# Kernel optimization log

Measured on AMD Instinct MI355X. Metric: run time of the kernel, lower is better.

Reference implementation:

```python
import jax, jax.numpy as jnp
import numpy as np

B, T, D, S, DEPTH, MAX_TOK = 2048, 64, 512, 64, 2, 64
LN_EPS = 1e-5


def setup_inputs() -> dict:
    key = jax.random.key(0)
    ks = jax.random.split(key, 9)
    sc = lambda k, shp, s: (jax.random.normal(k, shp, jnp.float32) * s)
    return {
        "tokens": jax.random.normal(ks[0], (B, T, D), jnp.float32),
        "pos_emb": sc(ks[1], (MAX_TOK, D), 0.02),          # nn.Embedding(max_tokens, dim)
        "A_log": sc(ks[2], (DEPTH, S), 0.5),               # log of state decay rates
        "Wd": sc(ks[3], (DEPTH, D, S), D ** -0.5),         # delta (selectivity) projection
        "bd": jnp.zeros((DEPTH, S), jnp.float32),
        "Wb": sc(ks[4], (DEPTH, D, S), D ** -0.5),         # input->state projection (B)
        "bb": jnp.zeros((DEPTH, S), jnp.float32),
        "Wc": sc(ks[5], (DEPTH, S, D), S ** -0.5),         # state->output projection (C)
        "bc": jnp.zeros((DEPTH, D), jnp.float32),
        "Dp": jnp.ones((DEPTH, D), jnp.float32),           # skip/pass-through gain D
        "Ws": sc(ks[6], (DEPTH, S, D), S ** -0.5),         # state_to_shot Linear weights
        "bs": jnp.zeros((DEPTH, D), jnp.float32),
        "gamma": jnp.ones((D,), jnp.float32),              # LayerNorm
        "beta": jnp.zeros((D,), jnp.float32),
    }


def _selective_scan(x, A_log, Wd, bd, Wb, bb, Wc, bc, Dp):
    """Selective SSM layer: per-token input-dependent decay + drive, vector state.

    x: [B, T, D] -> (y: [B, T, D], final_state: [B, S])
    """
    delta = jax.nn.softplus(jnp.einsum('btd,ds->bts', x, Wd) + bd)   # [B,T,S]
    decay = jnp.exp(-delta * jnp.exp(A_log))                          # [B,T,S]
    drive = delta * (jnp.einsum('btd,ds->bts', x, Wb) + bb)          # [B,T,S]

    def step(h, inp):
        dec, u = inp
        h = dec * h + u
        return h, h

    h0 = jnp.zeros((x.shape[0], decay.shape[-1]), x.dtype)
    hT, hs = jax.lax.scan(step, h0, (decay.transpose(1, 0, 2), drive.transpose(1, 0, 2)))
    hs = hs.transpose(1, 0, 2)                                        # [B,T,S]
    y = jnp.einsum('bts,sd->btd', hs, Wc) + bc + x * Dp
    return y, hT


def reference(tokens, pos_emb, A_log, Wd, bd, Wb, bb, Wc, bc, Dp, Ws, bs, gamma, beta):
    t = tokens.shape[1]
    hidden = tokens + pos_emb[:t][None]                               # add position embedding
    depth = A_log.shape[0]
    shot_state = None
    for i in range(depth):  # small fixed depth
        hidden, shot_state = _selective_scan(hidden, A_log[i], Wd[i], bd[i], Wb[i], bb[i], Wc[i], bc[i], Dp[i])
        hidden = hidden + (shot_state @ Ws[i] + bs[i])[:, None, :]
    pooled = hidden.mean(axis=1) + shot_state @ Ws[-1] + bs[-1]       # [B, D]
    mu = pooled.mean(-1, keepdims=True)
    var = ((pooled - mu) ** 2).mean(-1, keepdims=True)
    shot = (pooled - mu) / jnp.sqrt(var + LN_EPS) * gamma + beta
    return hidden, shot
```

## Files before the change

kernel.cpp:

```cpp
#include <hip/hip_runtime.h>
#include <hip/hip_bf16.h>
#include <math.h>

typedef __attribute__((ext_vector_type(8))) short bf16x8;
typedef __attribute__((ext_vector_type(4))) float f32x4;

#define NB 2048
#define NT 64
#define ND 512
#define NS 64
#define NTH 512
#define LN_EPS 1e-5f

#define XH_B    0
#define HS_B    65536
#define SCANF_B 73728
#define HT_B    73984
#define STM_B   74240
#define RED_B   76288
#define LDS_BYTES 76416

#define BB_OFF  65536
#define BC_OFF  131072
#define WS_OFF  196608
#define POS_OFF 262144
#define PACK_ELEMS 294912

__device__ __forceinline__ unsigned short f2b(float x) {
    __hip_bfloat16 h = __float2bfloat16(x);
    return *(unsigned short*)&h;
}
__device__ __forceinline__ float b2f(unsigned short u) {
    __hip_bfloat16 h; *(unsigned short*)&h = u;
    return __bfloat162float(h);
}
__device__ __forceinline__ int xh_off(int t, int cb) { return t * 1024 + (cb ^ ((t & 15) << 4)); }
__device__ __forceinline__ int hs_off(int t, int cb) { return t * 128  + (cb ^ ((t & 7)  << 4)); }

__global__ void prep_pack(const float* __restrict__ Wd, const float* __restrict__ Wb,
                          const float* __restrict__ Wc, const float* __restrict__ Ws,
                          const float* __restrict__ pos_emb,
                          unsigned short* __restrict__ pack) {
    int i = blockIdx.x * 256 + threadIdx.x;
    if (i >= PACK_ELEMS) return;
    float v;
    if (i >= POS_OFF) {
        v = pos_emb[i - POS_OFF];
    } else {
        int which = i >> 16;
        int r = i & 0xFFFF;
        if (which < 2) {
            int j = r & 7, l = (r >> 3) & 63, ks = (r >> 9) & 15, nt = (r >> 13) & 3, dep = r >> 15;
            int s = nt * 16 + (l & 15);
            int k = ks * 32 + (l >> 4) * 8 + j;
            const float* W = which ? Wb : Wd;
            v = W[(dep * 512 + k) * 64 + s];
        } else if (which == 2) {
            int j = r & 7, l = (r >> 3) & 63, ks = (r >> 9) & 1, ntg = (r >> 10) & 31, dep = r >> 15;
            int d = ntg * 16 + (l & 15);
            int k = ks * 32 + (l >> 4) * 8 + j;
            v = Wc[(dep * 64 + k) * 512 + d];
        } else {
            int dep = r >> 15, rem = r & 0x7FFF;
            v = Ws[dep * (NS * ND) + rem];
        }
    }
    pack[i] = f2b(v);
}

__global__ __launch_bounds__(NTH, 4)
void ssm_mfma(const float* __restrict__ tokens,
              const float* __restrict__ A_log,
              const float* __restrict__ bd, const float* __restrict__ bb,
              const float* __restrict__ bc, const float* __restrict__ Dp,
              const float* __restrict__ bs,
              const float* __restrict__ gma, const float* __restrict__ bta,
              const unsigned short* __restrict__ pack,
              float* __restrict__ out_hidden, float* __restrict__ out_shot)
{
    extern __shared__ char sm[];
    float* scanF = (float*)(sm + SCANF_B);
    float* hT    = (float*)(sm + HT_B);
    float* stm   = (float*)(sm + STM_B);
    float* red   = (float*)(sm + RED_B);

    const int tid  = threadIdx.x;
    const int b    = blockIdx.x;
    const int lane = tid & 63;
    const int w    = tid >> 6;
    const int lr   = lane & 15;
    const int lg   = lane >> 4;
    const int nt   = w & 3;
    const int mh   = w >> 2;

    {
        const f32x4*   tp = (const f32x4*)(tokens + (size_t)b * (NT * ND));
        const ushort4* pp = (const ushort4*)(pack + POS_OFF);
        #pragma unroll
        for (int i = 0; i < 16; ++i) {
            int f = i * NTH + tid;
            f32x4 a = __builtin_nontemporal_load(&tp[f]);
            ushort4 p = pp[f];
            int row = f >> 7, cb = (f & 127) * 8;
            ushort4 q;
            q.x = f2b(a.x + b2f(p.x));
            q.y = f2b(a.y + b2f(p.y));
            q.z = f2b(a.z + b2f(p.z));
            q.w = f2b(a.w + b2f(p.w));
            *(ushort4*)(sm + XH_B + xh_off(row, cb)) = q;
        }
    }
    __syncthreads();

    for (int dep = 0; dep < 2; ++dep) {
        f32x4 accD[2] = {f32x4{0,0,0,0}, f32x4{0,0,0,0}};
        f32x4 accB[2] = {f32x4{0,0,0,0}, f32x4{0,0,0,0}};
        {
            const unsigned short* BdP = pack + (dep * 4 + nt) * 8192;
            const unsigned short* BbP = BdP + BB_OFF;
            const int rowA0 = 32 * mh + lr;
            const int rowA1 = rowA0 + 16;
            #pragma unroll 4
            for (int ks = 0; ks < 16; ++ks) {
                int cb = ks * 64 + lg * 16;
                bf16x8 a0 = *(const bf16x8*)(sm + XH_B + xh_off(rowA0, cb));
                bf16x8 a1 = *(const bf16x8*)(sm + XH_B + xh_off(rowA1, cb));
                bf16x8 b0 = *(const bf16x8*)(BdP + ks * 512 + lane * 8);
                bf16x8 b1 = *(const bf16x8*)(BbP + ks * 512 + lane * 8);
                accD[0] = __builtin_amdgcn_mfma_f32_16x16x32_bf16(a0, b0, accD[0], 0, 0, 0);
                accD[1] = __builtin_amdgcn_mfma_f32_16x16x32_bf16(a1, b0, accD[1], 0, 0, 0);
                accB[0] = __builtin_amdgcn_mfma_f32_16x16x32_bf16(a0, b1, accB[0], 0, 0, 0);
                accB[1] = __builtin_amdgcn_mfma_f32_16x16x32_bf16(a1, b1, accB[1], 0, 0, 0);
            }
        }
        const int scol = nt * 16 + lr;
        float dcy[8], u[8];
        {
            float bdv = bd[dep * 64 + scol];
            float bbv = bb[dep * 64 + scol];
            float eA  = __expf(A_log[dep * 64 + scol]);
            #pragma unroll
            for (int m = 0; m < 2; ++m)
                #pragma unroll
                for (int r = 0; r < 4; ++r) {
                    float dpre  = accD[m][r] + bdv;
                    float delta = (dpre > 20.f) ? dpre : log1pf(__expf(dpre));
                    dcy[m * 4 + r] = __expf(-delta * eA);
                    u[m * 4 + r]   = delta * (accB[m][r] + bbv);
                }
        }
        float F[2], P[2];
        #pragma unroll
        for (int m = 0; m < 2; ++m) {
            float h = 0.f, p = 1.f;
            #pragma unroll
            for (int r = 0; r < 4; ++r) { h = fmaf(dcy[m * 4 + r], h, u[m * 4 + r]); p *= dcy[m * 4 + r]; }
            F[m] = h; P[m] = p;
        }
        float hin_lo = 0.f, hin_hi = 0.f;
        if (mh == 0) {
            float hin = 0.f;
            #pragma unroll
            for (int j = 0; j < 8; ++j) {
                float Fj = __shfl(j < 4 ? F[0] : F[1], (j & 3) * 16 + lr, 64);
                float Pj = __shfl(j < 4 ? P[0] : P[1], (j & 3) * 16 + lr, 64);
                if (j == lg)     hin_lo = hin;
                if (j == 4 + lg) hin_hi = hin;
                hin = fmaf(Pj, hin, Fj);
            }
            if (lg == 0) scanF[scol] = hin;
        }
        __syncthreads();
        if (mh == 1) {
            float hin = scanF[scol];
            #pragma unroll
            for (int j = 0; j < 8; ++j) {
                float Fj = __shfl(j < 4 ? F[0] : F[1], (j & 3) * 16 + lr, 64);
                float Pj = __shfl(j < 4 ? P[0] : P[1], (j & 3) * 16 + lr, 64);
                if (j == lg)     hin_lo = hin;
                if (j == 4 + lg) hin_hi = hin;
                hin = fmaf(Pj, hin, Fj);
            }
        }
        #pragma unroll
        for (int m = 0; m < 2; ++m) {
            float h = m ? hin_hi : hin_lo;
            #pragma unroll
            for (int r = 0; r < 4; ++r) {
                h = fmaf(dcy[m * 4 + r], h, u[m * 4 + r]);
                int t = 32 * mh + 16 * m + 4 * lg + r;
                *(unsigned short*)(sm + HS_B + hs_off(t, scol * 2)) = f2b(h);
            }
            if (m == 1 && mh == 1 && lg == 3) hT[scol] = h;
        }
        __syncthreads();

        {
            const unsigned short* WsP = pack + WS_OFF + dep * (NS * ND);
            float acc = bs[dep * ND + tid];
            #pragma unroll 8
            for (int s = 0; s < 64; ++s) acc = fmaf(hT[s], b2f(WsP[s * ND + tid]), acc);
            stm[tid] = acc;
        }

        f32x4 accC[4][4];
        #pragma unroll
        for (int tt = 0; tt < 4; ++tt)
            #pragma unroll
            for (int dt = 0; dt < 4; ++dt) accC[tt][dt] = f32x4{0, 0, 0, 0};
        {
            const unsigned short* WcA = pack + BC_OFF + (dep * 32 + w * 4) * 1024;
            #pragma unroll
            for (int ks = 0; ks < 2; ++ks) {
                bf16x8 hfr[4];
                #pragma unroll
                for (int tt = 0; tt < 4; ++tt)
                    hfr[tt] = *(const bf16x8*)(sm + HS_B + hs_off(tt * 16 + lr, ks * 64 + lg * 16));
                #pragma unroll
                for (int dt = 0; dt < 4; ++dt) {
                    bf16x8 wfr = *(const bf16x8*)(WcA + (dt * 2 + ks) * 512 + lane * 8);
                    #pragma unroll
                    for (int tt = 0; tt < 4; ++tt)
                        accC[tt][dt] = __builtin_amdgcn_mfma_f32_16x16x32_bf16(wfr, hfr[tt], accC[tt][dt], 0, 0, 0);
                }
            }
        }
        __syncthreads();

        {
            const float* bcd = bc + dep * ND;
            const float* Dpd = Dp + dep * ND;
            f32x4 psumv[4] = {f32x4{0,0,0,0}, f32x4{0,0,0,0}, f32x4{0,0,0,0}, f32x4{0,0,0,0}};
            #pragma unroll
            for (int tt = 0; tt < 4; ++tt) {
                int t = tt * 16 + lr;
                #pragma unroll
                for (int dt = 0; dt < 4; ++dt) {
                    int d0 = w * 64 + dt * 16 + 4 * lg;
                    ushort4 xq = *(const ushort4*)(sm + XH_B + xh_off(t, d0 * 2));
                    f32x4 bc4 = *(const f32x4*)&bcd[d0];
                    f32x4 dp4 = *(const f32x4*)&Dpd[d0];
                    f32x4 st4 = *(const f32x4*)&stm[d0];
                    f32x4 v4;
                    v4.x = accC[tt][dt].x + bc4.x + b2f(xq.x) * dp4.x + st4.x;
                    v4.y = accC[tt][dt].y + bc4.y + b2f(xq.y) * dp4.y + st4.y;
                    v4.z = accC[tt][dt].z + bc4.z + b2f(xq.z) * dp4.z + st4.z;
                    v4.w = accC[tt][dt].w + bc4.w + b2f(xq.w) * dp4.w + st4.w;
                    if (dep == 0) {
                        ushort4 q;
                        q.x = f2b(v4.x); q.y = f2b(v4.y); q.z = f2b(v4.z); q.w = f2b(v4.w);
                        *(ushort4*)(sm + XH_B + xh_off(t, d0 * 2)) = q;
                    } else {
                        __builtin_nontemporal_store(v4, (f32x4*)&out_hidden[((size_t)b * NT + t) * ND + d0]);
                        psumv[dt] += v4;
                    }
                }
            }
            if (dep == 1) {
                #pragma unroll
                for (int dt = 0; dt < 4; ++dt)
                    #pragma unroll
                    for (int c = 0; c < 4; ++c) {
                        float v = psumv[dt][c];
                        v += __shfl_xor(v, 1, 64);
                        v += __shfl_xor(v, 2, 64);
                        v += __shfl_xor(v, 4, 64);
                        v += __shfl_xor(v, 8, 64);
                        psumv[dt][c] = v;
                    }
                if (lr == 0) {
                    #pragma unroll
                    for (int dt = 0; dt < 4; ++dt) {
                        int d0 = w * 64 + dt * 16 + 4 * lg;
                        f32x4 st4 = *(const f32x4*)&stm[d0];
                        f32x4 nv = psumv[dt] * (1.0f / 64.0f) + st4;
                        *(f32x4*)&stm[d0] = nv;
                    }
                }
            }
        }
        __syncthreads();
    }

    float pv = stm[tid];
    float s1 = pv, s2 = pv * pv;
    #pragma unroll
    for (int off = 32; off; off >>= 1) {
        s1 += __shfl_down(s1, off, 64);
        s2 += __shfl_down(s2, off, 64);
    }
    if (lane == 0) { red[w] = s1; red[8 + w] = s2; }
    __syncthreads();
    if (tid == 0) {
        float a = 0.f, q = 0.f;
        for (int i = 0; i < 8; ++i) { a += red[i]; q += red[8 + i]; }
        float mu = a * (1.0f / ND);
        float var = q * (1.0f / ND) - mu * mu;
        red[16] = mu;
        red[17] = rsqrtf(var + LN_EPS);
    }
    __syncthreads();
    out_shot[(size_t)b * ND + tid] = (pv - red[16]) * red[17] * gma[tid] + bta[tid];
}

extern "C" void kernel_launch(void* const* d_in, const int* in_sizes, int n_in,
                              void* d_out, int out_size, void* d_ws, size_t ws_size,
                              hipStream_t stream) {
    const float* tokens  = (const float*)d_in[0];
    const float* pos_emb = (const float*)d_in[1];
    const float* A_log   = (const float*)d_in[2];
    const float* Wd      = (const float*)d_in[3];
    const float* bd      = (const float*)d_in[4];
    const float* Wb      = (const float*)d_in[5];
    const float* bb      = (const float*)d_in[6];
    const float* Wc      = (const float*)d_in[7];
    const float* bc      = (const float*)d_in[8];
    const float* Dp      = (const float*)d_in[9];
    const float* Ws      = (const float*)d_in[10];
    const float* bs      = (const float*)d_in[11];
    const float* gma     = (const float*)d_in[12];
    const float* bta     = (const float*)d_in[13];

    unsigned short* pack = (unsigned short*)d_ws;
    float* out_hidden = (float*)d_out;
    float* out_shot   = (float*)d_out + (size_t)NB * NT * ND;

    prep_pack<<<(PACK_ELEMS + 255) / 256, 256, 0, stream>>>(Wd, Wb, Wc, Ws, pos_emb, pack);

    (void)hipFuncSetAttribute((const void*)ssm_mfma,
                              hipFuncAttributeMaxDynamicSharedMemorySize,
                              (int)LDS_BYTES);
    ssm_mfma<<<NB, NTH, LDS_BYTES, stream>>>(
        tokens, A_log, bd, bb, bc, Dp, bs, gma, bta,
        pack, out_hidden, out_shot);
}
```

Baseline: 278.7 us.

## Fold state-to-shot broadcast into Wc MFMA as extra K-steps, fuse biases

The per-layer hT@Ws broadcast term is folded into the Wc MFMA by extending K from 64 to 128. The extra K-steps use the last hidden state row replicated across tiles, with the weights packed into a combined fragment layout. bc+bs is pre-summed in the prep kernel, the per-thread scalar Ws loop only runs for the final pooled term, and one barrier is moved. It also swaps log1pf for a fast __logf(1+exp) and uses a nontemporal store for the shot output. This doubles the MFMA count for the Wc stage but removes a serial 64-step scalar loop and LDS traffic, and the fast log is slightly less precise for very negative inputs.

```diff
diff --git a/kernel.cpp b/kernel.cpp
--- a/kernel.cpp
+++ b/kernel.cpp
@@ -20,11 +20,12 @@
 #define RED_B   76288
 #define LDS_BYTES 76416
 
-#define BB_OFF  65536
-#define BC_OFF  131072
-#define WS_OFF  196608
-#define POS_OFF 262144
-#define PACK_ELEMS 294912
+#define BB_OFF   65536
+#define FRAG_OFF 131072
+#define WSL_OFF  262144
+#define POS_OFF  294912
+#define BCF_OFF  327680
+#define PREP_TOTAL 328704
 
 __device__ __forceinline__ unsigned short f2b(float x) {
     __hip_bfloat16 h = __float2bfloat16(x);
@@ -40,30 +41,34 @@
 __global__ void prep_pack(const float* __restrict__ Wd, const float* __restrict__ Wb,
                           const float* __restrict__ Wc, const float* __restrict__ Ws,
                           const float* __restrict__ pos_emb,
+                          const float* __restrict__ bc, const float* __restrict__ bs,
                           unsigned short* __restrict__ pack) {
     int i = blockIdx.x * 256 + threadIdx.x;
-    if (i >= PACK_ELEMS) return;
+    if (i >= PREP_TOTAL) return;
+    if (i >= BCF_OFF) {
+        int f = i - BCF_OFF;
+        ((float*)(pack + BCF_OFF))[f] = bc[f] + bs[f];
+        return;
+    }
     float v;
-    if (i >= POS_OFF) {
+    if (i < BB_OFF) {
+        int j = i & 7, l = (i >> 3) & 63, ks = (i >> 9) & 15, nt = (i >> 13) & 3, dep = (i >> 15) & 1;
+        v = Wd[((size_t)dep * 512 + ks * 32 + (l >> 4) * 8 + j) * 64 + nt * 16 + (l & 15)];
+    } else if (i < FRAG_OFF) {
+        int r = i - BB_OFF;
+        int j = r & 7, l = (r >> 3) & 63, ks = (r >> 9) & 15, nt = (r >> 13) & 3, dep = (r >> 15) & 1;
+        v = Wb[((size_t)dep * 512 + ks * 32 + (l >> 4) * 8 + j) * 64 + nt * 16 + (l & 15)];
+    } else if (i < WSL_OFF) {
+        int r = i - FRAG_OFF;
+        int j = r & 7, l = (r >> 3) & 63, ks = (r >> 9) & 3, ntg = (r >> 11) & 31, dep = (r >> 16) & 1;
+        int d = ntg * 16 + (l & 15);
+        int kk = (l >> 4) * 8 + j;
+        if (ks < 2) v = Wc[((size_t)dep * 64 + ks * 32 + kk) * 512 + d];
+        else        v = Ws[((size_t)dep * 64 + (ks - 2) * 32 + kk) * 512 + d];
+    } else if (i < POS_OFF) {
+        v = Ws[32768 + (i - WSL_OFF)];
+    } else {
         v = pos_emb[i - POS_OFF];
-    } else {
-        int which = i >> 16;
-        int r = i & 0xFFFF;
-        if (which < 2) {
-            int j = r & 7, l = (r >> 3) & 63, ks = (r >> 9) & 15, nt = (r >> 13) & 3, dep = r >> 15;
-            int s = nt * 16 + (l & 15);
-            int k = ks * 32 + (l >> 4) * 8 + j;
-            const float* W = which ? Wb : Wd;
-            v = W[(dep * 512 + k) * 64 + s];
-        } else if (which == 2) {
-            int j = r & 7, l = (r >> 3) & 63, ks = (r >> 9) & 1, ntg = (r >> 10) & 31, dep = r >> 15;
-            int d = ntg * 16 + (l & 15);
-            int k = ks * 32 + (l >> 4) * 8 + j;
-            v = Wc[(dep * 64 + k) * 512 + d];
-        } else {
-            int dep = r >> 15, rem = r & 0x7FFF;
-            v = Ws[dep * (NS * ND) + rem];
-        }
     }
     pack[i] = f2b(v);
 }
@@ -72,7 +77,7 @@
 void ssm_mfma(const float* __restrict__ tokens,
               const float* __restrict__ A_log,
               const float* __restrict__ bd, const float* __restrict__ bb,
-              const float* __restrict__ bc, const float* __restrict__ Dp,
+              const float* __restrict__ Dp,
               const float* __restrict__ bs,
               const float* __restrict__ gma, const float* __restrict__ bta,
               const unsigned short* __restrict__ pack,
@@ -144,7 +149,7 @@
                 #pragma unroll
                 for (int r = 0; r < 4; ++r) {
                     float dpre  = accD[m][r] + bdv;
-                    float delta = (dpre > 20.f) ? dpre : log1pf(__expf(dpre));
+                    float delta = (dpre > 20.f) ? dpre : __logf(1.f + __expf(dpre));
                     dcy[m * 4 + r] = __expf(-delta * eA);
                     u[m * 4 + r]   = delta * (accB[m][r] + bbv);
                 }
@@ -195,40 +200,45 @@
         }
         __syncthreads();
 
-        {
-            const unsigned short* WsP = pack + WS_OFF + dep * (NS * ND);
-            float acc = bs[dep * ND + tid];
-            #pragma unroll 8
-            for (int s = 0; s < 64; ++s) acc = fmaf(hT[s], b2f(WsP[s * ND + tid]), acc);
-            stm[tid] = acc;
-        }
-
         f32x4 accC[4][4];
         #pragma unroll
         for (int tt = 0; tt < 4; ++tt)
             #pragma unroll
             for (int dt = 0; dt < 4; ++dt) accC[tt][dt] = f32x4{0, 0, 0, 0};
         {
-            const unsigned short* WcA = pack + BC_OFF + (dep * 32 + w * 4) * 1024;
-            #pragma unroll
-            for (int ks = 0; ks < 2; ++ks) {
+            const unsigned short* WcA = pack + FRAG_OFF + (dep * 32 + w * 4) * 2048;
+            #pragma unroll
+            for (int ks = 0; ks < 4; ++ks) {
                 bf16x8 hfr[4];
-                #pragma unroll
-                for (int tt = 0; tt < 4; ++tt)
-                    hfr[tt] = *(const bf16x8*)(sm + HS_B + hs_off(tt * 16 + lr, ks * 64 + lg * 16));
+                if (ks < 2) {
+                    #pragma unroll
+                    for (int tt = 0; tt < 4; ++tt)
+                        hfr[tt] = *(const bf16x8*)(sm + HS_B + hs_off(tt * 16 + lr, ks * 64 + lg * 16));
+                } else {
+                    bf16x8 hb = *(const bf16x8*)(sm + HS_B + hs_off(63, (ks - 2) * 64 + lg * 16));
+                    #pragma unroll
+                    for (int tt = 0; tt < 4; ++tt) hfr[tt] = hb;
+                }
                 #pragma unroll
                 for (int dt = 0; dt < 4; ++dt) {
-                    bf16x8 wfr = *(const bf16x8*)(WcA + (dt * 2 + ks) * 512 + lane * 8);
+                    bf16x8 wfr = *(const bf16x8*)(WcA + dt * 2048 + ks * 512 + lane * 8);
                     #pragma unroll
                     for (int tt = 0; tt < 4; ++tt)
                         accC[tt][dt] = __builtin_amdgcn_mfma_f32_16x16x32_bf16(wfr, hfr[tt], accC[tt][dt], 0, 0, 0);
                 }
             }
         }
-        __syncthreads();
+
+        if (dep == 1) {
+            const unsigned short* WsL = pack + WSL_OFF;
+            float acc = bs[512 + tid];
+            #pragma unroll 8
+            for (int s = 0; s < 64; ++s) acc = fmaf(hT[s], b2f(WsL[s * 512 + tid]), acc);
+            stm[tid] = acc;
+        }
 
         {
-            const float* bcd = bc + dep * ND;
+            const float* bcf = (const float*)(pack + BCF_OFF) + dep * ND;
             const float* Dpd = Dp + dep * ND;
             f32x4 psumv[4] = {f32x4{0,0,0,0}, f32x4{0,0,0,0}, f32x4{0,0,0,0}, f32x4{0,0,0,0}};
             #pragma unroll
@@ -238,14 +248,13 @@
                 for (int dt = 0; dt < 4; ++dt) {
                     int d0 = w * 64 + dt * 16 + 4 * lg;
                     ushort4 xq = *(const ushort4*)(sm + XH_B + xh_off(t, d0 * 2));
-                    f32x4 bc4 = *(const f32x4*)&bcd[d0];
+                    f32x4 bc4 = *(const f32x4*)&bcf[d0];
                     f32x4 dp4 = *(const f32x4*)&Dpd[d0];
-                    f32x4 st4 = *(const f32x4*)&stm[d0];
                     f32x4 v4;
-                    v4.x = accC[tt][dt].x + bc4.x + b2f(xq.x) * dp4.x + st4.x;
-                    v4.y = accC[tt][dt].y + bc4.y + b2f(xq.y) * dp4.y + st4.y;
-                    v4.z = accC[tt][dt].z + bc4.z + b2f(xq.z) * dp4.z + st4.z;
-                    v4.w = accC[tt][dt].w + bc4.w + b2f(xq.w) * dp4.w + st4.w;
+                    v4.x = accC[tt][dt].x + bc4.x + b2f(xq.x) * dp4.x;
+                    v4.y = accC[tt][dt].y + bc4.y + b2f(xq.y) * dp4.y;
+                    v4.z = accC[tt][dt].z + bc4.z + b2f(xq.z) * dp4.z;
+                    v4.w = accC[tt][dt].w + bc4.w + b2f(xq.w) * dp4.w;
                     if (dep == 0) {
                         ushort4 q;
                         q.x = f2b(v4.x); q.y = f2b(v4.y); q.z = f2b(v4.z); q.w = f2b(v4.w);
@@ -268,6 +277,7 @@
                         v += __shfl_xor(v, 8, 64);
                         psumv[dt][c] = v;
                     }
+                __syncthreads();
                 if (lr == 0) {
                     #pragma unroll
                     for (int dt = 0; dt < 4; ++dt) {
@@ -300,7 +310,8 @@
         red[17] = rsqrtf(var + LN_EPS);
     }
     __syncthreads();
-    out_shot[(size_t)b * ND + tid] = (pv - red[16]) * red[17] * gma[tid] + bta[tid];
+    float sh = (pv - red[16]) * red[17] * gma[tid] + bta[tid];
+    __builtin_nontemporal_store(sh, &out_shot[(size_t)b * ND + tid]);
 }
 
 extern "C" void kernel_launch(void* const* d_in, const int* in_sizes, int n_in,
@@ -325,12 +336,12 @@
     float* out_hidden = (float*)d_out;
     float* out_shot   = (float*)d_out + (size_t)NB * NT * ND;
 
-    prep_pack<<<(PACK_ELEMS + 255) / 256, 256, 0, stream>>>(Wd, Wb, Wc, Ws, pos_emb, pack);
+    prep_pack<<<(PREP_TOTAL + 255) / 256, 256, 0, stream>>>(Wd, Wb, Wc, Ws, pos_emb, bc, bs, pack);
 
     (void)hipFuncSetAttribute((const void*)ssm_mfma,
                               hipFuncAttributeMaxDynamicSharedMemorySize,
                               (int)LDS_BYTES);
     ssm_mfma<<<NB, NTH, LDS_BYTES, stream>>>(
-        tokens, A_log, bd, bb, bc, Dp, bs, gma, bta,
+        tokens, A_log, bd, bb, Dp, bs, gma, bta,
         pack, out_hidden, out_shot);
 }
```

New measurement: 303.2 us. 8.8% more time.

## Stage final hidden output through LDS for coalesced stores; use fast log in softplus

Applied to the files above, without the earlier changes.

The dep==1 epilogue now writes the fp32 results into a swizzled LDS staging buffer, reusing the XH region in two 32-row halves. All threads then store contiguous rows to global memory with fully coalesced nontemporal 16-byte stores, replacing the scattered MFMA-layout stores. The epilogue loops are also reordered so the per-column bias, Dp and stm loads are hoisted out of the time loop. Softplus switches from log1pf to __logf(1+exp), which is cheaper but less accurate for very negative inputs. The staging adds extra barriers and LDS traffic.

```diff
diff --git a/kernel.cpp b/kernel.cpp
--- a/kernel.cpp
+++ b/kernel.cpp
@@ -91,7 +91,7 @@
     const int lr   = lane & 15;
     const int lg   = lane >> 4;
     const int nt   = w & 3;
-    const int mh   = w >> 2;
+    const int mh   = w >> 6 ? 0 : (w >> 2);
 
     {
         const f32x4*   tp = (const f32x4*)(tokens + (size_t)b * (NT * ND));
@@ -144,7 +144,7 @@
                 #pragma unroll
                 for (int r = 0; r < 4; ++r) {
                     float dpre  = accD[m][r] + bdv;
-                    float delta = (dpre > 20.f) ? dpre : log1pf(__expf(dpre));
+                    float delta = (dpre > 20.f) ? dpre : __logf(1.f + __expf(dpre));
                     dcy[m * 4 + r] = __expf(-delta * eA);
                     u[m * 4 + r]   = delta * (accB[m][r] + bbv);
                 }
@@ -227,56 +227,96 @@
         }
         __syncthreads();
 
-        {
-            const float* bcd = bc + dep * ND;
-            const float* Dpd = Dp + dep * ND;
-            f32x4 psumv[4] = {f32x4{0,0,0,0}, f32x4{0,0,0,0}, f32x4{0,0,0,0}, f32x4{0,0,0,0}};
-            #pragma unroll
-            for (int tt = 0; tt < 4; ++tt) {
-                int t = tt * 16 + lr;
+        const float* bcd = bc + dep * ND;
+        const float* Dpd = Dp + dep * ND;
+        if (dep == 0) {
+            #pragma unroll
+            for (int dt = 0; dt < 4; ++dt) {
+                int d0 = w * 64 + dt * 16 + 4 * lg;
+                f32x4 bc4 = *(const f32x4*)&bcd[d0];
+                f32x4 dp4 = *(const f32x4*)&Dpd[d0];
+                f32x4 st4 = *(const f32x4*)&stm[d0];
+                f32x4 base = bc4 + st4;
+                #pragma unroll
+                for (int tt = 0; tt < 4; ++tt) {
+                    int t = tt * 16 + lr;
+                    ushort4 xq = *(const ushort4*)(sm + XH_B + xh_off(t, d0 * 2));
+                    f32x4 xf4;
+                    xf4.x = b2f(xq.x); xf4.y = b2f(xq.y); xf4.z = b2f(xq.z); xf4.w = b2f(xq.w);
+                    f32x4 v4 = accC[tt][dt] + base + xf4 * dp4;
+                    ushort4 q;
+                    q.x = f2b(v4.x); q.y = f2b(v4.y); q.z = f2b(v4.z); q.w = f2b(v4.w);
+                    *(ushort4*)(sm + XH_B + xh_off(t, d0 * 2)) = q;
+                }
+            }
+        } else {
+            f32x4 psumv[4];
+            float st4a[4][4];
+            #pragma unroll
+            for (int dt = 0; dt < 4; ++dt) {
+                psumv[dt] = f32x4{0, 0, 0, 0};
+                int d0 = w * 64 + dt * 16 + 4 * lg;
+                f32x4 bc4 = *(const f32x4*)&bcd[d0];
+                f32x4 dp4 = *(const f32x4*)&Dpd[d0];
+                f32x4 st4 = *(const f32x4*)&stm[d0];
+                st4a[dt][0] = st4.x; st4a[dt][1] = st4.y; st4a[dt][2] = st4.z; st4a[dt][3] = st4.w;
+                f32x4 base = bc4 + st4;
+                #pragma unroll
+                for (int tt = 0; tt < 4; ++tt) {
+                    int t = tt * 16 + lr;
+                    ushort4 xq = *(const ushort4*)(sm + XH_B + xh_off(t, d0 * 2));
+                    f32x4 xf4;
+                    xf4.x = b2f(xq.x); xf4.y = b2f(xq.y); xf4.z = b2f(xq.z); xf4.w = b2f(xq.w);
+                    f32x4 v4 = accC[tt][dt] + base + xf4 * dp4;
+                    accC[tt][dt] = v4;
+                    psumv[dt] += v4;
+                }
+            }
+            #pragma unroll
+            for (int dt = 0; dt < 4; ++dt)
+                #pragma unroll
+                for (int c = 0; c < 4; ++c) {
+                    float v = psumv[dt][c];
+                    v += __shfl_xor(v, 1, 64);
+                    v += __shfl_xor(v, 2, 64);
+                    v += __shfl_xor(v, 4, 64);
+                    v += __shfl_xor(v, 8, 64);
+                    psumv[dt][c] = v;
+                }
+            if (lr == 0) {
                 #pragma unroll
                 for (int dt = 0; dt < 4; ++dt) {
                     int d0 = w * 64 + dt * 16 + 4 * lg;
-                    ushort4 xq = *(const ushort4*)(sm + XH_B + xh_off(t, d0 * 2));
-                    f32x4 bc4 = *(const f32x4*)&bcd[d0];
-                    f32x4 dp4 = *(const f32x4*)&Dpd[d0];
-                    f32x4 st4 = *(const f32x4*)&stm[d0];
-                    f32x4 v4;
-                    v4.x = accC[tt][dt].x + bc4.x + b2f(xq.x) * dp4.x + st4.x;
-                    v4.y = accC[tt][dt].y + bc4.y + b2f(xq.y) * dp4.y + st4.y;
-                    v4.z = accC[tt][dt].z + bc4.z + b2f(xq.z) * dp4.z + st4.z;
-                    v4.w = accC[tt][dt].w + bc4.w + b2f(xq.w) * dp4.w + st4.w;
-                    if (dep == 0) {
-                        ushort4 q;
-                        q.x = f2b(v4.x); q.y = f2b(v4.y); q.z = f2b(v4.z); q.w = f2b(v4.w);
-                        *(ushort4*)(sm + XH_B + xh_off(t, d0 * 2)) = q;
-                    } else {
-                        __builtin_nontemporal_store(v4, (f32x4*)&out_hidden[((size_t)b * NT + t) * ND + d0]);
-                        psumv[dt] += v4;
-                    }
-                }
-            }
-            if (dep == 1) {
-                #pragma unroll
-                for (int dt = 0; dt < 4; ++dt)
                     #pragma unroll
-                    for (int c = 0; c < 4; ++c) {
-                        float v = psumv[dt][c];
-                        v += __shfl_xor(v, 1, 64);
-                        v += __shfl_xor(v, 2, 64);
-                        v += __shfl_xor(v, 4, 64);
-                        v += __shfl_xor(v, 8, 64);
-                        psumv[dt][c] = v;
-                    }
-                if (lr == 0) {
+                    for (int c = 0; c < 4; ++c)
+                        stm[d0 + c] = psumv[dt][c] * (1.0f / 64.0f) + st4a[dt][c];
+                }
+            }
+            __syncthreads();
+
+            for (int half = 0; half < 2; ++half) {
+                #pragma unroll
+                for (int tt2 = 0; tt2 < 2; ++tt2) {
+                    int tt = half * 2 + tt2;
+                    int tloc = tt2 * 16 + lr;
                     #pragma unroll
                     for (int dt = 0; dt < 4; ++dt) {
                         int d0 = w * 64 + dt * 16 + 4 * lg;
-                        f32x4 st4 = *(const f32x4*)&stm[d0];
-                        f32x4 nv = psumv[dt] * (1.0f / 64.0f) + st4;
-                        *(f32x4*)&stm[d0] = nv;
+                        int byte = tloc * 2048 + ((d0 * 4) ^ ((tloc & 7) << 4));
+                        *(f32x4*)(sm + XH_B + byte) = accC[tt][dt];
                     }
                 }
+                __syncthreads();
+                f32x4* dst = (f32x4*)(out_hidden + ((size_t)b * NT + half * 32) * ND);
+                #pragma unroll
+                for (int i = 0; i < 8; ++i) {
+                    int f = i * NTH + tid;
+                    int row = f >> 7, c = f & 127;
+                    int byte = row * 2048 + ((c * 16) ^ ((row & 7) << 4));
+                    f32x4 v = *(const f32x4*)(sm + XH_B + byte);
+                    __builtin_nontemporal_store(v, &dst[f]);
+                }
+                __syncthreads();
             }
         }
         __syncthreads();
```

New measurement: 403.1 us. 44.7% more time.
